# Optimization experiments

Measured on AMD Instinct MI355X. Metric: run time of the kernel, lower is better.

Reference implementation:

```python
import jax, jax.numpy as jnp
import numpy as np

NUM_IMU = 72
NUM_NOISE = 12
MAX_PROP = 300
LN_EPS = 1e-5

def _softplus(x):
    return jax.nn.softplus(x)

def setup_inputs() -> dict:
    key = jax.random.key(0)
    k1, k2, k3, k4, k5 = jax.random.split(key, 5)
    d_model = 1024
    seq_len = 4096
    hidden_states = jax.random.normal(k1, (1, seq_len, d_model), dtype=jnp.float32)
    ln_gamma = jnp.ones((d_model,), dtype=jnp.float32)
    ln_beta = jnp.zeros((d_model,), dtype=jnp.float32)
    # Linear: d_model -> NUM_IMU * NUM_NOISE
    W = jax.random.normal(k2, (d_model, NUM_IMU * NUM_NOISE), dtype=jnp.float32) / np.sqrt(d_model)
    b = jax.random.normal(k3, (NUM_IMU * NUM_NOISE,), dtype=jnp.float32) * 0.01
    return {"hidden_states": hidden_states, "ln_gamma": ln_gamma, "ln_beta": ln_beta, "W": W, "b": b}

def _forward(hidden_states, ln_gamma, ln_beta, W, b):
    seq_len = hidden_states.shape[1]
    tsteps = min(MAX_PROP, seq_len)
    x = hidden_states[0]  # [seq, d_model] (squeeze batch=1)
    mu = jnp.mean(x, axis=-1, keepdims=True)
    var = jnp.mean((x - mu) ** 2, axis=-1, keepdims=True)
    xn = (x - mu) * jax.lax.rsqrt(var + LN_EPS) * ln_gamma + ln_beta
    # noise params: [seq, NUM_NOISE, NUM_IMU]
    p = (xn @ W + b).reshape(seq_len, NUM_NOISE, NUM_IMU)
    c = p[:, 4, :]
    c_theta = p[:, 5, :]
    phi = p[:, 6, :]
    phi_theta = p[:, 7, :]
    d = _softplus(p[:, 1, :])
    k = d ** 2 / 4 + _softplus(p[:, 0, :])
    d_theta = _softplus(p[:, 3, :])
    k_theta = d_theta ** 2 / 4 + _softplus(p[:, 2, :])
    acc_base = p[:, 8, :].T      # [imu, seq]
    acc_std = _softplus(p[:, 9, :]).T
    gyro_base = p[:, 10, :].T
    gyro_std = _softplus(p[:, 11, :]).T
    # vectorize over imu: move to [imu, seq, 1]
    def I(a):
        return a.T[:, :, None]
    t = jnp.arange(tsteps, dtype=jnp.float32)[None, None, :]  # [1,1,tstep]
    k_, d_, phi_, c_ = I(k), I(d), I(phi), I(c)
    kt_, dt_, pht_, ct_ = I(k_theta), I(d_theta), I(phi_theta), I(c_theta)
    omega1 = jnp.sqrt(k_ * 4 - d_ ** 2) / 2
    lin = c_ * jnp.exp(-d_ / 2 * t) * jnp.sin(t * omega1 + phi_)
    omega2 = jnp.sqrt(kt_ * 4 - dt_ ** 2) / 2
    ang = ct_ * jnp.exp(-dt_ / 2 * t) * jnp.sin(t * omega2 + pht_)
    spring = lin + ang  # [imu, seq, tstep]
    # banded scatter-add: out[s+t] += spring[:, s, t] for s+t < seq_len
    pos = jnp.arange(seq_len, dtype=jnp.int32)[:, None] + jnp.arange(tsteps, dtype=jnp.int32)[None, :]
    pos_flat = pos.reshape(-1)
    mask = pos_flat < seq_len
    pos_safe = jnp.where(mask, pos_flat, 0)
    vals = spring.reshape(NUM_IMU, -1) * mask.astype(spring.dtype)
    kinematics = jnp.zeros((NUM_IMU, seq_len), dtype=spring.dtype).at[:, pos_safe].add(vals)
    return kinematics, acc_base, acc_std, gyro_base, gyro_std

def reference(hidden_states, ln_gamma, ln_beta, W, b):
    return _forward(hidden_states, ln_gamma, ln_beta, W, b)
```

## Files before the change

kernel.cpp:

```cpp
#include <hip/hip_runtime.h>
#include <hip/hip_bf16.h>
#include <math.h>

#define SEQ 4096
#define DM  1024
#define NIMU 72
#define NNOISE 12
#define NJ (NIMU*NNOISE)
#define TSTEPS 300
#define PLANE (NIMU*SEQ)

#define A2F_SHORTS ((size_t)128 * 128 * 512)
#define BTF_SHORTS ((size_t)28 * 128 * 512)

typedef __attribute__((ext_vector_type(8))) short bf16x8;
typedef __attribute__((ext_vector_type(16))) float f32x16;
typedef __attribute__((ext_vector_type(4))) float f32x4;
typedef __attribute__((ext_vector_type(2))) float f32x2;

__device__ __forceinline__ float softplus_f(float x) {
    return fmaxf(x, 0.f) + log1pf(expf(-fabsf(x)));
}

__device__ __forceinline__ void split_bf16(float x, short& hi, short& lo) {
    unsigned b = __float_as_uint(x);
    unsigned h = (b + 0x7FFFu + ((b >> 16) & 1u)) >> 16;
    float hf = __uint_as_float(h << 16);
    float r = x - hf;
    unsigned b2 = __float_as_uint(r);
    unsigned l2 = (b2 + 0x7FFFu + ((b2 >> 16) & 1u)) >> 16;
    hi = (short)h;
    lo = (short)l2;
}

__device__ __forceinline__ void gload_lds16(const void* g, void* l) {
    __builtin_amdgcn_global_load_lds(
        (const __attribute__((address_space(1))) unsigned int*)g,
        (__attribute__((address_space(3))) unsigned int*)l,
        16, 0, 0);
}

__global__ __launch_bounds__(512) void ln_kernel(const float* __restrict__ x,
                                                 const float* __restrict__ gamma,
                                                 const float* __restrict__ beta,
                                                 short* __restrict__ A2f) {
    const int tid = threadIdx.x;
    const int row = blockIdx.x * 16 + (tid >> 5);
    const int c   = tid & 31;
    const float4* xr = (const float4*)(x + (size_t)row * DM);

    float s = 0.f, sq = 0.f;
    #pragma unroll
    for (int i = 0; i < 8; ++i) {
        float4 v = xr[c + 32 * i];
        s  += v.x + v.y + v.z + v.w;
        sq += v.x*v.x + v.y*v.y + v.z*v.z + v.w*v.w;
    }
    #pragma unroll
    for (int off = 1; off < 32; off <<= 1) {
        s  += __shfl_xor(s, off);
        sq += __shfl_xor(sq, off);
    }
    const float mean = s * (1.f / DM);
    const float var  = sq * (1.f / DM) - mean * mean;
    const float rstd = rsqrtf(fmaxf(var, 0.f) + 1e-5f);

    const int s_tile = row >> 5, r = row & 31;
    #pragma unroll
    for (int i = 0; i < 8; ++i) {
        const int c4 = c + 32 * i;
        float4 v  = xr[c4];
        float4 gm = ((const float4*)gamma)[c4];
        float4 bt = ((const float4*)beta)[c4];
        float o[4];
        o[0] = (v.x - mean) * rstd * gm.x + bt.x;
        o[1] = (v.y - mean) * rstd * gm.y + bt.y;
        o[2] = (v.z - mean) * rstd * gm.z + bt.z;
        o[3] = (v.w - mean) * rstd * gm.w + bt.w;
        short4 hv, lv;
        split_bf16(o[0], hv.x, lv.x);
        split_bf16(o[1], hv.y, lv.y);
        split_bf16(o[2], hv.z, lv.z);
        split_bf16(o[3], hv.w, lv.w);
        const int ch = c4 >> 2;
        const int g  = (c4 >> 1) & 1;
        const int o4 = (c4 & 1) * 4;
        const size_t base = ((size_t)s_tile * 128 + ch) * 512 + (g * 32 + r) * 8 + o4;
        *(short4*)(A2f + base)                    = hv;
        *(short4*)(A2f + base + (size_t)64 * 512) = lv;
    }
}

__global__ __launch_bounds__(256) void wprep_kernel(const float* __restrict__ W,
                                                    short* __restrict__ Btf) {
    __shared__ float T[32][33];
    const int k0 = blockIdx.x * 32, j0 = blockIdx.y * 32;
    const int t = threadIdx.x;
    {
        const int r = t >> 3, c4 = (t & 7) * 4;
        float4 v = *(const float4*)(W + (size_t)(k0 + r) * NJ + j0 + c4);
        T[r][c4 + 0] = v.x; T[r][c4 + 1] = v.y; T[r][c4 + 2] = v.z; T[r][c4 + 3] = v.w;
    }
    __syncthreads();
    if (t < 128) {
        const int q = t >> 6;
        const int l = t & 63;
        const int n = l & 31, g = l >> 5;
        const int jt = blockIdx.y;
        const int ch = blockIdx.x * 2 + q;
        bf16x8 hv, lv;
        #pragma unroll
        for (int o = 0; o < 8; ++o) {
            short h, lo_;
            split_bf16(T[q * 16 + g * 8 + o][n], h, lo_);
            hv[o] = h; lv[o] = lo_;
        }
        short* dh = Btf + ((size_t)jt * 128 + ch) * 512 + l * 8;
        *(bf16x8*)dh = hv;
        *(bf16x8*)(dh + (size_t)64 * 512) = lv;
    }
}

__global__ __launch_bounds__(256, 2) void gemm_kernel(const short* __restrict__ A2f,
                                                      const short* __restrict__ Btf,
                                                      const float* __restrict__ bias,
                                                      float* __restrict__ ptA,
                                                      float* __restrict__ ptB) {
    __shared__ bf16x8 lds[2][32][64];

    const int bid = blockIdx.x;
    const int c = bid & 7, u = bid >> 3;
    const int kh = u / 28, v = u - kh * 28;
    const int bxi = v / 7, by = v - bxi * 7;
    const int bx = c * 4 + bxi;
    const int l = threadIdx.x & 63, w = threadIdx.x >> 6;
    const int bx4 = bx * 4, by4 = by * 4;
    const int mt0 = bx4 + (w & 1) * 2;
    const int jt0 = by4 + (w >> 1) * 2;
    const int ch0 = kh * 32;

    const int schl = w >> 1;
    const bool sA  = (w & 1) == 0;

    auto stage = [&](int buf, int it) {
        const int ch = ch0 + it * 2 + schl;
        #pragma unroll
        for (int i = 0; i < 8; ++i) {
            const int tt = i >> 1, part = i & 1;
            const short* src = sA
                ? A2f + ((size_t)(bx4 + tt) * 128 + ch + part * 64) * 512 + l * 8
                : Btf + ((size_t)(by4 + tt) * 128 + ch + part * 64) * 512 + l * 8;
            gload_lds16(src, &lds[buf][schl * 16 + (sA ? 0 : 8) + i][0]);
        }
    };

    f32x16 acc[2][2] = {};
    const int wa = (w & 1) * 2;
    const int wb = (w >> 1) * 2;

    stage(0, 0);
    __syncthreads();

    for (int it = 0; it < 16; ++it) {
        const int cur = it & 1;
        if (it + 1 < 16) stage(cur ^ 1, it + 1);
        #pragma unroll
        for (int chl = 0; chl < 2; ++chl) {
            const int gb = chl * 16;
            bf16x8 a0h = lds[cur][gb + (wa + 0) * 2 + 0][l];
            bf16x8 a0l = lds[cur][gb + (wa + 0) * 2 + 1][l];
            bf16x8 a1h = lds[cur][gb + (wa + 1) * 2 + 0][l];
            bf16x8 a1l = lds[cur][gb + (wa + 1) * 2 + 1][l];
            bf16x8 b0h = lds[cur][gb + 8 + (wb + 0) * 2 + 0][l];
            bf16x8 b0l = lds[cur][gb + 8 + (wb + 0) * 2 + 1][l];
            bf16x8 b1h = lds[cur][gb + 8 + (wb + 1) * 2 + 0][l];
            bf16x8 b1l = lds[cur][gb + 8 + (wb + 1) * 2 + 1][l];
            acc[0][0] = __builtin_amdgcn_mfma_f32_32x32x16_bf16(a0h, b0h, acc[0][0], 0, 0, 0);
            acc[0][1] = __builtin_amdgcn_mfma_f32_32x32x16_bf16(a0h, b1h, acc[0][1], 0, 0, 0);
            acc[1][0] = __builtin_amdgcn_mfma_f32_32x32x16_bf16(a1h, b0h, acc[1][0], 0, 0, 0);
            acc[1][1] = __builtin_amdgcn_mfma_f32_32x32x16_bf16(a1h, b1h, acc[1][1], 0, 0, 0);
            acc[0][0] = __builtin_amdgcn_mfma_f32_32x32x16_bf16(a0h, b0l, acc[0][0], 0, 0, 0);
            acc[0][1] = __builtin_amdgcn_mfma_f32_32x32x16_bf16(a0h, b1l, acc[0][1], 0, 0, 0);
            acc[1][0] = __builtin_amdgcn_mfma_f32_32x32x16_bf16(a1h, b0l, acc[1][0], 0, 0, 0);
            acc[1][1] = __builtin_amdgcn_mfma_f32_32x32x16_bf16(a1h, b1l, acc[1][1], 0, 0, 0);
            acc[0][0] = __builtin_amdgcn_mfma_f32_32x32x16_bf16(a0l, b0h, acc[0][0], 0, 0, 0);
            acc[0][1] = __builtin_amdgcn_mfma_f32_32x32x16_bf16(a0l, b1h, acc[0][1], 0, 0, 0);
            acc[1][0] = __builtin_amdgcn_mfma_f32_32x32x16_bf16(a1l, b0h, acc[1][0], 0, 0, 0);
            acc[1][1] = __builtin_amdgcn_mfma_f32_32x32x16_bf16(a1l, b1h, acc[1][1], 0, 0, 0);
        }
        __syncthreads();
    }

    float* ptH = kh ? ptB : ptA;
    const int jn = l & 31, hi5 = l >> 5;
    #pragma unroll
    for (int ni = 0; ni < 2; ++ni) {
        const int jt = jt0 + ni;
        if (jt < 27) {
            const int j = jt * 32 + jn;
            const float bj = (kh == 0) ? bias[j] : 0.f;
            #pragma unroll
            for (int mi = 0; mi < 2; ++mi) {
                #pragma unroll
                for (int q = 0; q < 4; ++q) {
                    f32x4 o;
                    o[0] = acc[mi][ni][q * 4 + 0] + bj;
                    o[1] = acc[mi][ni][q * 4 + 1] + bj;
                    o[2] = acc[mi][ni][q * 4 + 2] + bj;
                    o[3] = acc[mi][ni][q * 4 + 3] + bj;
                    const int s = (mt0 + mi) * 32 + q * 8 + hi5 * 4;
                    *(f32x4*)(ptH + (size_t)j * SEQ + s) = o;
                }
            }
        }
    }
}

__global__ __launch_bounds__(256) void spring_kernel(const float* __restrict__ ptA,
                                                     const float* __restrict__ ptB,
                                                     float* __restrict__ kin) {
    __shared__ float w3[3][4 * 368];
    const int tid  = threadIdx.x;
    const int lane = tid & 63;
    const int wid  = tid >> 6;
    const int s0   = blockIdx.x * 256;
    const int imu  = blockIdx.y;
    const int s    = s0 + (wid << 6) + lane;

    #pragma unroll
    for (int b = 0; b < 3; ++b)
        #pragma unroll
        for (int i = 0; i < 6; ++i) {
            const int idx = lane + i * 64;
            if (idx < 363) w3[b][wid * 368 + idx] = 0.f;
        }

    const int base = imu * SEQ + s;
    const float p0  = ptA[(size_t)0 * PLANE + base] + ptB[(size_t)0 * PLANE + base];
    const float p1  = ptA[(size_t)1 * PLANE + base] + ptB[(size_t)1 * PLANE + base];
    const float p2  = ptA[(size_t)2 * PLANE + base] + ptB[(size_t)2 * PLANE + base];
    const float p3  = ptA[(size_t)3 * PLANE + base] + ptB[(size_t)3 * PLANE + base];
    const float c1  = ptA[(size_t)4 * PLANE + base] + ptB[(size_t)4 * PLANE + base];
    const float c2  = ptA[(size_t)5 * PLANE + base] + ptB[(size_t)5 * PLANE + base];
    const float ph1 = ptA[(size_t)6 * PLANE + base] + ptB[(size_t)6 * PLANE + base];
    const float ph2 = ptA[(size_t)7 * PLANE + base] + ptB[(size_t)7 * PLANE + base];

    float dd = softplus_f(p1);
    float kk = dd * dd * 0.25f + softplus_f(p0);
    float om1 = 0.5f * sqrtf(fmaxf(4.f * kk - dd * dd, 0.f));
    float dt = softplus_f(p3);
    float kt = dt * dt * 0.25f + softplus_f(p2);
    float om2 = 0.5f * sqrtf(fmaxf(4.f * kt - dt * dt, 0.f));
    float e1 = expf(-0.5f * dd), e2 = expf(-0.5f * dt);
    float sn, cs, sn2, cs2;
    sincosf(om1, &sn, &cs);
    sincosf(om2, &sn2, &cs2);
    f32x2 Rr = {e1 * cs, e2 * cs2};
    f32x2 Ri = {e1 * sn, e2 * sn2};
    sincosf(ph1, &sn, &cs);
    sincosf(ph2, &sn2, &cs2);
    f32x2 zr = {c1 * cs, c2 * cs2};
    f32x2 zi = {c1 * sn, c2 * sn2};

    f32x2 zrB, ziB;
    {
        f32x2 prr = Rr, pri = Ri;
        f32x2 qr = {1.f, 1.f}, qi = {0.f, 0.f};
        int e = 150;
        while (e) {
            if (e & 1) {
                f32x2 nr = qr * prr - qi * pri;
                qi = qr * pri + qi * prr;
                qr = nr;
            }
            f32x2 nr = prr * prr - pri * pri;
            pri = 2.f * prr * pri;
            prr = nr;
            e >>= 1;
        }
        f32x2 nr = zr * qr - zi * qi;
        ziB = zr * qi + zi * qr;
        zrB = nr;
    }

    float* q0 = &w3[0][wid * 368 + lane];
    float* q1 = &w3[1][wid * 368 + lane];
    float* q2 = &w3[2][wid * 368 + lane];

    #pragma unroll 1
    for (int j = 0; j < 150; j += 3) {
        float vA0 = zi.x + zi.y;
        { f32x2 nr = zr * Rr - zi * Ri; zi = zr * Ri + zi * Rr; zr = nr; }
        float vA1 = zi.x + zi.y;
        { f32x2 nr = zr * Rr - zi * Ri; zi = zr * Ri + zi * Rr; zr = nr; }
        float vA2 = zi.x + zi.y;
        { f32x2 nr = zr * Rr - zi * Ri; zi = zr * Ri + zi * Rr; zr = nr; }
        float vB0 = ziB.x + ziB.y;
        { f32x2 nr = zrB * Rr - ziB * Ri; ziB = zrB * Ri + ziB * Rr; zrB = nr; }
        float vB1 = ziB.x + ziB.y;
        { f32x2 nr = zrB * Rr - ziB * Ri; ziB = zrB * Ri + ziB * Rr; zrB = nr; }
        float vB2 = ziB.x + ziB.y;
        { f32x2 nr = zrB * Rr - ziB * Ri; ziB = zrB * Ri + ziB * Rr; zrB = nr; }

        const float a0 = q0[j],     b0 = q0[j + 150];
        const float a1 = q1[j + 1], b1 = q1[j + 151];
        const float a2 = q2[j + 2], b2 = q2[j + 152];
        q0[j]       = a0 + vA0;  q0[j + 150] = b0 + vB0;
        q1[j + 1]   = a1 + vA1;  q1[j + 151] = b1 + vB1;
        q2[j + 2]   = a2 + vA2;  q2[j + 152] = b2 + vB2;
        __asm__ volatile("" ::: "memory");
    }

    __syncthreads();
    for (int i = tid; i < 555; i += 256) {
        float sum = 0.f;
        #pragma unroll
        for (int w = 0; w < 4; ++w) {
            const int idx = i - (w << 6);
            if (idx >= 0 && idx < 363) {
                const int o = w * 368 + idx;
                sum += w3[0][o] + w3[1][o] + w3[2][o];
            }
        }
        const int pos = s0 + i;
        if (pos < SEQ) {
            (void)__hip_atomic_fetch_add(&kin[(size_t)imu * SEQ + pos], sum,
                                         __ATOMIC_RELAXED, __HIP_MEMORY_SCOPE_AGENT);
        }
    }
}

__global__ __launch_bounds__(256) void tail_kernel(const float* __restrict__ ptA,
                                                   const float* __restrict__ ptB,
                                                   float* __restrict__ out) {
    const int i4 = blockIdx.x * 256 + threadIdx.x;
    if (i4 >= PLANE) return;
    const float4 a = ((const float4*)(ptA + (size_t)8 * PLANE))[i4];
    const float4 b = ((const float4*)(ptB + (size_t)8 * PLANE))[i4];
    float4 v;
    v.x = a.x + b.x; v.y = a.y + b.y; v.z = a.z + b.z; v.w = a.w + b.w;
    const int q = (int)(((size_t)i4 * 4) / PLANE);
    if (q & 1) {
        v.x = softplus_f(v.x); v.y = softplus_f(v.y);
        v.z = softplus_f(v.z); v.w = softplus_f(v.w);
    }
    ((float4*)(out + (size_t)PLANE))[i4] = v;
}

extern "C" void kernel_launch(void* const* d_in, const int* in_sizes, int n_in,
                              void* d_out, int out_size, void* d_ws, size_t ws_size,
                              hipStream_t stream) {
    const float* hs    = (const float*)d_in[0];
    const float* gamma = (const float*)d_in[1];
    const float* beta  = (const float*)d_in[2];
    const float* W     = (const float*)d_in[3];
    const float* b     = (const float*)d_in[4];
    float* out = (float*)d_out;

    short* A2f = (short*)d_ws;
    short* Btf = A2f + A2F_SHORTS;
    float* ptA = (float*)(Btf + BTF_SHORTS);
    float* ptB = ptA + (size_t)12 * PLANE;

    hipMemsetAsync(out, 0, (size_t)PLANE * sizeof(float), stream);

    ln_kernel<<<SEQ / 16, 512, 0, stream>>>(hs, gamma, beta, A2f);
    wprep_kernel<<<dim3(DM / 32, NJ / 32), 256, 0, stream>>>(W, Btf);
    gemm_kernel<<<448, 256, 0, stream>>>(A2f, Btf, b, ptA, ptB);
    spring_kernel<<<dim3(SEQ / 256, NIMU), 256, 0, stream>>>(ptA, ptB, out);
    tail_kernel<<<(PLANE + 255) / 256, 256, 0, stream>>>(ptA, ptB, out);
}
```

Baseline: 138.7 us.

## Deepen GEMM LDS pipeline to four stages and fuse tail into spring kernel

The GEMM main loop moves from a double-buffered 2-chunk-per-iteration scheme to a 4-deep ring of single-chunk LDS buffers, using explicit vmcnt waits and raw barriers to keep three loads in flight while computing. All four waves now share the staging work evenly instead of splitting A and B by wave. The separate tail kernel is removed, and the spring kernel now also writes the four base/std output planes with softplus, saving one launch and one pass over those planes. The hand-written waitcnt counts depend on exactly how many loads each stage issues, so a mismatch could race.

```diff
diff --git a/kernel.cpp b/kernel.cpp
--- a/kernel.cpp
+++ b/kernel.cpp
@@ -126,7 +126,7 @@
                                                       const float* __restrict__ bias,
                                                       float* __restrict__ ptA,
                                                       float* __restrict__ ptB) {
-    __shared__ bf16x8 lds[2][32][64];
+    __shared__ bf16x8 lds[4][16][64];
 
     const int bid = blockIdx.x;
     const int c = bid & 7, u = bid >> 3;
@@ -139,18 +139,20 @@
     const int jt0 = by4 + (w >> 1) * 2;
     const int ch0 = kh * 32;
 
-    const int schl = w >> 1;
-    const bool sA  = (w & 1) == 0;
-
     auto stage = [&](int buf, int it) {
-        const int ch = ch0 + it * 2 + schl;
+        const int ch = ch0 + it;
         #pragma unroll
-        for (int i = 0; i < 8; ++i) {
-            const int tt = i >> 1, part = i & 1;
-            const short* src = sA
-                ? A2f + ((size_t)(bx4 + tt) * 128 + ch + part * 64) * 512 + l * 8
-                : Btf + ((size_t)(by4 + tt) * 128 + ch + part * 64) * 512 + l * 8;
-            gload_lds16(src, &lds[buf][schl * 16 + (sA ? 0 : 8) + i][0]);
+        for (int i = 0; i < 4; ++i) {
+            const int slot = w * 4 + i;
+            const short* src;
+            if (slot < 8) {
+                const int tt = slot >> 1, part = slot & 1;
+                src = A2f + ((size_t)(bx4 + tt) * 128 + ch + part * 64) * 512 + l * 8;
+            } else {
+                const int tt = (slot - 8) >> 1, part = slot & 1;
+                src = Btf + ((size_t)(by4 + tt) * 128 + ch + part * 64) * 512 + l * 8;
+            }
+            gload_lds16(src, &lds[buf][slot][0]);
         }
     };
 
@@ -158,38 +160,47 @@
     const int wa = (w & 1) * 2;
     const int wb = (w >> 1) * 2;
 
-    stage(0, 0);
-    __syncthreads();
-
-    for (int it = 0; it < 16; ++it) {
-        const int cur = it & 1;
-        if (it + 1 < 16) stage(cur ^ 1, it + 1);
-        #pragma unroll
-        for (int chl = 0; chl < 2; ++chl) {
-            const int gb = chl * 16;
-            bf16x8 a0h = lds[cur][gb + (wa + 0) * 2 + 0][l];
-            bf16x8 a0l = lds[cur][gb + (wa + 0) * 2 + 1][l];
-            bf16x8 a1h = lds[cur][gb + (wa + 1) * 2 + 0][l];
-            bf16x8 a1l = lds[cur][gb + (wa + 1) * 2 + 1][l];
-            bf16x8 b0h = lds[cur][gb + 8 + (wb + 0) * 2 + 0][l];
-            bf16x8 b0l = lds[cur][gb + 8 + (wb + 0) * 2 + 1][l];
-            bf16x8 b1h = lds[cur][gb + 8 + (wb + 1) * 2 + 0][l];
-            bf16x8 b1l = lds[cur][gb + 8 + (wb + 1) * 2 + 1][l];
-            acc[0][0] = __builtin_amdgcn_mfma_f32_32x32x16_bf16(a0h, b0h, acc[0][0], 0, 0, 0);
-            acc[0][1] = __builtin_amdgcn_mfma_f32_32x32x16_bf16(a0h, b1h, acc[0][1], 0, 0, 0);
-            acc[1][0] = __builtin_amdgcn_mfma_f32_32x32x16_bf16(a1h, b0h, acc[1][0], 0, 0, 0);
-            acc[1][1] = __builtin_amdgcn_mfma_f32_32x32x16_bf16(a1h, b1h, acc[1][1], 0, 0, 0);
-            acc[0][0] = __builtin_amdgcn_mfma_f32_32x32x16_bf16(a0h, b0l, acc[0][0], 0, 0, 0);
-            acc[0][1] = __builtin_amdgcn_mfma_f32_32x32x16_bf16(a0h, b1l, acc[0][1], 0, 0, 0);
-            acc[1][0] = __builtin_amdgcn_mfma_f32_32x32x16_bf16(a1h, b0l, acc[1][0], 0, 0, 0);
-            acc[1][1] = __builtin_amdgcn_mfma_f32_32x32x16_bf16(a1h, b1l, acc[1][1], 0, 0, 0);
-            acc[0][0] = __builtin_amdgcn_mfma_f32_32x32x16_bf16(a0l, b0h, acc[0][0], 0, 0, 0);
-            acc[0][1] = __builtin_amdgcn_mfma_f32_32x32x16_bf16(a0l, b1h, acc[0][1], 0, 0, 0);
-            acc[1][0] = __builtin_amdgcn_mfma_f32_32x32x16_bf16(a1l, b0h, acc[1][0], 0, 0, 0);
-            acc[1][1] = __builtin_amdgcn_mfma_f32_32x32x16_bf16(a1l, b1h, acc[1][1], 0, 0, 0);
-        }
-        __syncthreads();
-    }
+    auto compute = [&](int cur) {
+        bf16x8 a0h = lds[cur][(wa + 0) * 2 + 0][l];
+        bf16x8 a0l = lds[cur][(wa + 0) * 2 + 1][l];
+        bf16x8 a1h = lds[cur][(wa + 1) * 2 + 0][l];
+        bf16x8 a1l = lds[cur][(wa + 1) * 2 + 1][l];
+        bf16x8 b0h = lds[cur][8 + (wb + 0) * 2 + 0][l];
+        bf16x8 b0l = lds[cur][8 + (wb + 0) * 2 + 1][l];
+        bf16x8 b1h = lds[cur][8 + (wb + 1) * 2 + 0][l];
+        bf16x8 b1l = lds[cur][8 + (wb + 1) * 2 + 1][l];
+        acc[0][0] = __builtin_amdgcn_mfma_f32_32x32x16_bf16(a0h, b0h, acc[0][0], 0, 0, 0);
+        acc[0][1] = __builtin_amdgcn_mfma_f32_32x32x16_bf16(a0h, b1h, acc[0][1], 0, 0, 0);
+        acc[1][0] = __builtin_amdgcn_mfma_f32_32x32x16_bf16(a1h, b0h, acc[1][0], 0, 0, 0);
+        acc[1][1] = __builtin_amdgcn_mfma_f32_32x32x16_bf16(a1h, b1h, acc[1][1], 0, 0, 0);
+        acc[0][0] = __builtin_amdgcn_mfma_f32_32x32x16_bf16(a0h, b0l, acc[0][0], 0, 0, 0);
+        acc[0][1] = __builtin_amdgcn_mfma_f32_32x32x16_bf16(a0h, b1l, acc[0][1], 0, 0, 0);
+        acc[1][0] = __builtin_amdgcn_mfma_f32_32x32x16_bf16(a1h, b0l, acc[1][0], 0, 0, 0);
+        acc[1][1] = __builtin_amdgcn_mfma_f32_32x32x16_bf16(a1h, b1l, acc[1][1], 0, 0, 0);
+        acc[0][0] = __builtin_amdgcn_mfma_f32_32x32x16_bf16(a0l, b0h, acc[0][0], 0, 0, 0);
+        acc[0][1] = __builtin_amdgcn_mfma_f32_32x32x16_bf16(a0l, b1h, acc[0][1], 0, 0, 0);
+        acc[1][0] = __builtin_amdgcn_mfma_f32_32x32x16_bf16(a1l, b0h, acc[1][0], 0, 0, 0);
+        acc[1][1] = __builtin_amdgcn_mfma_f32_32x32x16_bf16(a1l, b1h, acc[1][1], 0, 0, 0);
+    };
+
+    stage(0, 0); stage(1, 1); stage(2, 2);
+
+    #pragma unroll 1
+    for (int it = 0; it < 30; ++it) {
+        asm volatile("s_waitcnt vmcnt(8)" ::: "memory");
+        __builtin_amdgcn_s_barrier();
+        __builtin_amdgcn_sched_barrier(0);
+        if (it + 3 < 32) stage((it + 3) & 3, it + 3);
+        compute(it & 3);
+    }
+    asm volatile("s_waitcnt vmcnt(4)" ::: "memory");
+    __builtin_amdgcn_s_barrier();
+    __builtin_amdgcn_sched_barrier(0);
+    compute(30 & 3);
+    asm volatile("s_waitcnt vmcnt(0)" ::: "memory");
+    __builtin_amdgcn_s_barrier();
+    __builtin_amdgcn_sched_barrier(0);
+    compute(31 & 3);
 
     float* ptH = kh ? ptB : ptA;
     const int jn = l & 31, hi5 = l >> 5;
@@ -218,14 +229,14 @@
 
 __global__ __launch_bounds__(256) void spring_kernel(const float* __restrict__ ptA,
                                                      const float* __restrict__ ptB,
-                                                     float* __restrict__ kin) {
+                                                     float* __restrict__ out) {
     __shared__ float w3[3][4 * 368];
     const int tid  = threadIdx.x;
     const int lane = tid & 63;
     const int wid  = tid >> 6;
     const int s0   = blockIdx.x * 256;
     const int imu  = blockIdx.y;
-    const int s    = s0 + (wid << 6) + lane;
+    const int s    = s0 + tid;
 
     #pragma unroll
     for (int b = 0; b < 3; ++b)
@@ -311,6 +322,14 @@
         __asm__ volatile("" ::: "memory");
     }
 
+    #pragma unroll
+    for (int np = 0; np < 4; ++np) {
+        float v = ptA[(size_t)(8 + np) * PLANE + base]
+                + ptB[(size_t)(8 + np) * PLANE + base];
+        if (np & 1) v = softplus_f(v);
+        out[(size_t)(np + 1) * PLANE + base] = v;
+    }
+
     __syncthreads();
     for (int i = tid; i < 555; i += 256) {
         float sum = 0.f;
@@ -324,27 +343,10 @@
         }
         const int pos = s0 + i;
         if (pos < SEQ) {
-            (void)__hip_atomic_fetch_add(&kin[(size_t)imu * SEQ + pos], sum,
+            (void)__hip_atomic_fetch_add(&out[(size_t)imu * SEQ + pos], sum,
                                          __ATOMIC_RELAXED, __HIP_MEMORY_SCOPE_AGENT);
         }
     }
-}
-
-__global__ __launch_bounds__(256) void tail_kernel(const float* __restrict__ ptA,
-                                                   const float* __restrict__ ptB,
-                                                   float* __restrict__ out) {
-    const int i4 = blockIdx.x * 256 + threadIdx.x;
-    if (i4 >= PLANE) return;
-    const float4 a = ((const float4*)(ptA + (size_t)8 * PLANE))[i4];
-    const float4 b = ((const float4*)(ptB + (size_t)8 * PLANE))[i4];
-    float4 v;
-    v.x = a.x + b.x; v.y = a.y + b.y; v.z = a.z + b.z; v.w = a.w + b.w;
-    const int q = (int)(((size_t)i4 * 4) / PLANE);
-    if (q & 1) {
-        v.x = softplus_f(v.x); v.y = softplus_f(v.y);
-        v.z = softplus_f(v.z); v.w = softplus_f(v.w);
-    }
-    ((float4*)(out + (size_t)PLANE))[i4] = v;
 }
 
 extern "C" void kernel_launch(void* const* d_in, const int* in_sizes, int n_in,
@@ -368,5 +370,4 @@
     wprep_kernel<<<dim3(DM / 32, NJ / 32), 256, 0, stream>>>(W, Btf);
     gemm_kernel<<<448, 256, 0, stream>>>(A2f, Btf, b, ptA, ptB);
     spring_kernel<<<dim3(SEQ / 256, NIMU), 256, 0, stream>>>(ptA, ptB, out);
-    tail_kernel<<<(PLANE + 255) / 256, 256, 0, stream>>>(ptA, ptB, out);
-}
+}
```

Result: no change. 140.6 us (+1.4%).
